# Kernel tuning notes

Hardware: AMD Instinct MI355X
Metric: run time of the kernel (lower is better)

Reference implementation:

```python
import jax, jax.numpy as jnp
import numpy as np

SCALE = 0.08838834764831845  # 1/sqrt(128)
NEG_INF = -1e30


def setup_inputs() -> dict:
    key = jax.random.key(0)
    ks = jax.random.split(key, 6)
    S, Hq, Hkv, D, NB, BS, BMAX, X = 32, 32, 8, 128, 4096, 16, 128, 8
    query = jax.random.normal(ks[0], (S, Hq, D), jnp.float32)
    key_cache = jax.random.normal(ks[1], (NB, Hkv, D // X, BS, X), jnp.float32)
    value_cache = jax.random.normal(ks[2], (NB, Hkv, D, BS), jnp.float32)
    block_tables = jax.random.randint(ks[3], (S, BMAX), 0, NB, dtype=jnp.int32)
    seq_lens = jax.random.randint(ks[4], (S,), 1, BMAX * BS + 1, dtype=jnp.int32)
    alibi_slopes = jax.random.uniform(ks[5], (Hq,), jnp.float32)
    query_start_len = jnp.arange(S + 1, dtype=jnp.int32)  # every seq is a 1-token decode
    return dict(query_ptr=query, key_cache_ptr=key_cache, value_cache_ptr=value_cache,
                block_tables_ptr=block_tables, seq_lens_ptr=seq_lens,
                alibi_slopes_ptr=alibi_slopes, query_start_len_ptr=query_start_len)


def reference(query_ptr, key_cache_ptr, value_cache_ptr, block_tables_ptr,
              seq_lens_ptr, alibi_slopes_ptr, query_start_len_ptr):
    S, Bmax = block_tables_ptr.shape
    NB, Hkv, D0, BS, X = key_cache_ptr.shape
    D = D0 * X
    Hq = query_ptr.shape[1]
    G = Hq // Hkv  # queries per kv head
    Kmax = Bmax * BS

    # de-interleave vLLM K layout [NB,Hkv,D//x,BS,x] -> [NB,Hkv,BS,D]; K[d] = cache[.., d//x, tok, d%x]
    K = key_cache_ptr.transpose(0, 1, 3, 2, 4).reshape(NB, Hkv, BS, D).astype(jnp.float32)
    V = value_cache_ptr.transpose(0, 1, 3, 2).astype(jnp.float32)  # [NB,Hkv,BS,D]

    qstart = query_start_len_ptr[:-1]
    qlen = query_start_len_ptr[1:] - qstart

    q = query_ptr[qstart].astype(jnp.float32).reshape(S, Hkv, G, D)  # one decode token per seq

    # block-table-driven KV gather: [S,Bmax,Hkv,BS,D] -> [S,Hkv,Kmax,D]
    Kg = K[block_tables_ptr].transpose(0, 2, 1, 3, 4).reshape(S, Hkv, Kmax, D)
    Vg = V[block_tables_ptr].transpose(0, 2, 1, 3, 4).reshape(S, Hkv, Kmax, D)

    scores = SCALE * jnp.einsum('shgd,shkd->shgk', q, Kg)  # [S,Hkv,G,Kmax]

    pos = jnp.arange(Kmax, dtype=jnp.float32)
    ctx = (seq_lens_ptr.astype(jnp.float32) - 1.0)[:, None, None, None]
    slopes = alibi_slopes_ptr.reshape(Hkv, G)  # head idx = kv_head*G + q
    bias = slopes[None, :, :, None] * (pos[None, None, None, :] - ctx)
    valid = (jnp.arange(Kmax)[None, :] < seq_lens_ptr[:, None])[:, None, None, :]
    scores = jnp.where(valid, scores + bias, NEG_INF)

    m = jnp.max(scores, axis=-1, keepdims=True)
    p = jnp.exp(scores - m) * valid  # online-softmax numerator
    l = jnp.sum(p, axis=-1, keepdims=True)
    acc = jnp.einsum('shgk,shkd->shgd', p, Vg)
    out = acc / (l + 1e-10)  # matches acc/(L + 1e-10) in source

    decode = (qlen == 1).astype(query_ptr.dtype)  # seqs with query_len>1 are skipped (zeros)
    out = out.reshape(S, Hq, D).astype(query_ptr.dtype) * decode[:, None, None]
    return jnp.zeros_like(query_ptr).at[qstart].set(out)
```

## Files before the change

kernel.cpp:

```cpp
#include <hip/hip_runtime.h>

#define SCALE_F 0.08838834764831845f
#define NEG_INF -1e30f

constexpr int S    = 32;
constexpr int Hq   = 32;
constexpr int Hkv  = 8;
constexpr int G    = 4;
constexpr int D    = 128;
constexpr int BS   = 16;
constexpr int BMAX = 128;
constexpr int KMAX = BMAX * BS;

template<int PARTS>
__global__ __launch_bounds__(256, 4)
void attn_wave_kernel(const float* __restrict__ q_ptr,
                      const float* __restrict__ kc,
                      const float* __restrict__ vc,
                      const int*   __restrict__ bt,
                      const int*   __restrict__ slens,
                      const float* __restrict__ slopes,
                      float* __restrict__ part_acc,
                      float* __restrict__ part_m,
                      float* __restrict__ part_l)
{
    constexpr int CHUNKW = KMAX / PARTS;
    constexpr int NCH    = CHUNKW / 64;
    constexpr int CPW    = CHUNKW / BS;

    __shared__ float sm_p[4][G * CHUNKW];

    const int wid  = threadIdx.x >> 6;
    const int lane = threadIdx.x & 63;
    const int gw   = blockIdx.x * 4 + wid;
    const int part = gw % PARTS;
    const int sh   = gw / PARTS;
    const int h    = sh & (Hkv - 1);
    const int s    = sh >> 3;

    const int seq_len   = slens[s];
    const int num_parts = (seq_len + CHUNKW - 1) / CHUNKW;
    if (part >= num_parts) return;

    float* smp = sm_p[wid];

    int phys[CPW];
    #pragma unroll
    for (int i = 0; i < CPW; ++i) phys[i] = bt[s * BMAX + part * CPW + i];

    const float ctx  = (float)(seq_len - 1);
    const int   pos0 = part * CHUNKW;

    const int o4 = lane >> 4;
    const int t  = lane & 15;

    const float wslope = slopes[h * G + (t & 3)];

    float4 qa[G], qb[G];
    #pragma unroll
    for (int g = 0; g < G; ++g) {
        const float* qp = q_ptr + ((size_t)(s * Hq + h * G + g) * D + t * 8);
        qa[g] = ((const float4*)qp)[0];
        qb[g] = ((const float4*)qp)[1];
    }

    #pragma unroll
    for (int c = 0; c < NCH; ++c) {
        #pragma unroll
        for (int jb = 0; jb < 4; ++jb) {
            const float* kbase = kc + ((((size_t)phys[c * 4 + jb] * Hkv + h) * (D / 8) + t) * BS) * 8;
            float4 kA[4], kB[4];
            #pragma unroll
            for (int j2 = 0; j2 < 4; ++j2) {
                const float* kp = kbase + (j2 * 4 + o4) * 8;
                kA[j2] = ((const float4*)kp)[0];
                kB[j2] = ((const float4*)kp)[1];
            }
            #pragma unroll
            for (int j2 = 0; j2 < 4; ++j2) {
                float sc0 = qa[0].x*kA[j2].x + qa[0].y*kA[j2].y + qa[0].z*kA[j2].z + qa[0].w*kA[j2].w
                          + qb[0].x*kB[j2].x + qb[0].y*kB[j2].y + qb[0].z*kB[j2].z + qb[0].w*kB[j2].w;
                float sc1 = qa[1].x*kA[j2].x + qa[1].y*kA[j2].y + qa[1].z*kA[j2].z + qa[1].w*kA[j2].w
                          + qb[1].x*kB[j2].x + qb[1].y*kB[j2].y + qb[1].z*kB[j2].z + qb[1].w*kB[j2].w;
                float sc2 = qa[2].x*kA[j2].x + qa[2].y*kA[j2].y + qa[2].z*kA[j2].z + qa[2].w*kA[j2].w
                          + qb[2].x*kB[j2].x + qb[2].y*kB[j2].y + qb[2].z*kB[j2].z + qb[2].w*kB[j2].w;
                float sc3 = qa[3].x*kA[j2].x + qa[3].y*kA[j2].y + qa[3].z*kA[j2].z + qa[3].w*kA[j2].w
                          + qb[3].x*kB[j2].x + qb[3].y*kB[j2].y + qb[3].z*kB[j2].z + qb[3].w*kB[j2].w;
                #pragma unroll
                for (int msk = 8; msk >= 1; msk >>= 1) {
                    sc0 += __shfl_xor(sc0, msk, 16);
                    sc1 += __shfl_xor(sc1, msk, 16);
                    sc2 += __shfl_xor(sc2, msk, 16);
                    sc3 += __shfl_xor(sc3, msk, 16);
                }
                if (t < 4) {
                    const int pl   = c * 64 + (jb * 4 + j2) * 4 + o4;
                    const int kpos = pos0 + pl;
                    const float scv = (t == 0) ? sc0 : (t == 1) ? sc1 : (t == 2) ? sc2 : sc3;
                    smp[t * CHUNKW + pl] =
                        (kpos < seq_len) ? (SCALE_F * scv + wslope * ((float)kpos - ctx)) : NEG_INF;
                }
            }
        }
    }

    const int d0 = lane;
    float4 vreg[2][2][4];
    {
        const float* vb = vc + ((size_t)phys[0] * Hkv + h) * D * BS;
        #pragma unroll
        for (int c = 0; c < 4; ++c) {
            vreg[0][0][c] = ((const float4*)(vb + (size_t)d0 * BS))[c];
            vreg[0][1][c] = ((const float4*)(vb + (size_t)(d0 + 64) * BS))[c];
        }
    }

    {
        const int gS = lane >> 4;
        const int u  = lane & 15;
        float* rowp = smp + gS * CHUNKW;

        float4 sv[NCH];
        float m = NEG_INF;
        #pragma unroll
        for (int w = 0; w < NCH; ++w) {
            sv[w] = ((const float4*)(rowp + u * 4 + w * 64))[0];
            m = fmaxf(m, fmaxf(fmaxf(sv[w].x, sv[w].y), fmaxf(sv[w].z, sv[w].w)));
        }
        #pragma unroll
        for (int msk = 8; msk >= 1; msk >>= 1) m = fmaxf(m, __shfl_xor(m, msk, 16));

        float l = 0.f;
        #pragma unroll
        for (int w = 0; w < NCH; ++w) {
            float4 pv;
            pv.x = __expf(sv[w].x - m);
            pv.y = __expf(sv[w].y - m);
            pv.z = __expf(sv[w].z - m);
            pv.w = __expf(sv[w].w - m);
            l += pv.x + pv.y + pv.z + pv.w;
            ((float4*)(rowp + u * 4 + w * 64))[0] = pv;
        }
        #pragma unroll
        for (int msk = 8; msk >= 1; msk >>= 1) l += __shfl_xor(l, msk, 16);

        if (u == 0) {
            part_m[(sh * PARTS + part) * G + gS] = m;
            part_l[(sh * PARTS + part) * G + gS] = l;
        }
    }

    float acc0[G] = {0.f, 0.f, 0.f, 0.f};
    float acc1[G] = {0.f, 0.f, 0.f, 0.f};

    #pragma unroll
    for (int i = 0; i < CPW; ++i) {
        const int cb = i & 1;
        if (i + 1 < CPW) {
            const float* vb = vc + ((size_t)phys[i + 1] * Hkv + h) * D * BS;
            #pragma unroll
            for (int c = 0; c < 4; ++c) {
                vreg[cb ^ 1][0][c] = ((const float4*)(vb + (size_t)d0 * BS))[c];
                vreg[cb ^ 1][1][c] = ((const float4*)(vb + (size_t)(d0 + 64) * BS))[c];
            }
        }
        #pragma unroll
        for (int g = 0; g < G; ++g) {
            const float4* pp = (const float4*)(smp + g * CHUNKW + i * BS);
            #pragma unroll
            for (int c = 0; c < 4; ++c) {
                const float4 p4 = pp[c];
                acc0[g] += p4.x * vreg[cb][0][c].x + p4.y * vreg[cb][0][c].y
                         + p4.z * vreg[cb][0][c].z + p4.w * vreg[cb][0][c].w;
                acc1[g] += p4.x * vreg[cb][1][c].x + p4.y * vreg[cb][1][c].y
                         + p4.z * vreg[cb][1][c].z + p4.w * vreg[cb][1][c].w;
            }
        }
    }

    float* outp = part_acc + (size_t)(sh * PARTS + part) * G * D;
    #pragma unroll
    for (int g = 0; g < G; ++g) {
        outp[g * D + d0]      = acc0[g];
        outp[g * D + d0 + 64] = acc1[g];
    }
}

__global__ __launch_bounds__(512)
void attn_reduce_kernel(const float* __restrict__ part_acc,
                        const float* __restrict__ part_m,
                        const float* __restrict__ part_l,
                        const int*   __restrict__ slens,
                        float* __restrict__ out,
                        int parts, int chunk)
{
    const int sh  = blockIdx.x;
    const int s   = sh / Hkv;
    const int tid = threadIdx.x;
    const int g   = tid >> 7;
    const int d   = tid & 127;

    const int seq_len = slens[s];
    const int np = min(parts, (seq_len + chunk - 1) / chunk);

    float M = NEG_INF;
    for (int p = 0; p < np; ++p)
        M = fmaxf(M, part_m[(sh * parts + p) * G + g]);
    float L = 0.f, acc = 0.f;
    for (int p = 0; p < np; ++p) {
        const float w = __expf(part_m[(sh * parts + p) * G + g] - M);
        L += w * part_l[(sh * parts + p) * G + g];
        acc += w * part_acc[((size_t)(sh * parts + p) * G + g) * D + d];
    }
    out[(size_t)(sh * G + g) * D + d] = acc / (L + 1e-10f);
}

extern "C" void kernel_launch(void* const* d_in, const int* in_sizes, int n_in,
                              void* d_out, int out_size, void* d_ws, size_t ws_size,
                              hipStream_t stream)
{
    const float* q   = (const float*)d_in[0];
    const float* kc  = (const float*)d_in[1];
    const float* vc  = (const float*)d_in[2];
    const int*   bt  = (const int*)d_in[3];
    const int*   sl  = (const int*)d_in[4];
    const float* slp = (const float*)d_in[5];

    auto ws_need = [](int p) {
        return (size_t)S * Hkv * p * G * (D + 2) * sizeof(float);
    };
    int parts = 16;
    while (parts > 4 && ws_need(parts) > ws_size) parts >>= 1;
    const int chunk = KMAX / parts;

    float* part_acc = (float*)d_ws;
    float* part_m   = part_acc + (size_t)S * Hkv * parts * G * D;
    float* part_l   = part_m   + (size_t)S * Hkv * parts * G;

    const dim3 grid1(S * Hkv * parts / 4);
    switch (parts) {
    case 16: attn_wave_kernel<16><<<grid1, 256, 0, stream>>>(q, kc, vc, bt, sl, slp, part_acc, part_m, part_l); break;
    case 8:  attn_wave_kernel<8> <<<grid1, 256, 0, stream>>>(q, kc, vc, bt, sl, slp, part_acc, part_m, part_l); break;
    default: attn_wave_kernel<4> <<<grid1, 256, 0, stream>>>(q, kc, vc, bt, sl, slp, part_acc, part_m, part_l); break;
    }
    attn_reduce_kernel<<<S * Hkv, 512, 0, stream>>>(
        part_acc, part_m, part_l, sl, (float*)d_out, parts, chunk);
}
```

Before: 472.6 us.

## Double-buffer K block loads and split KV sequence into 32 partitions

The QK score loop now walks one 16-token cache block at a time and loads the next block's K vectors into a second register buffer while the current block is computed, so global-load latency overlaps with the FMAs. The default split count rises from 16 to 32, which gives 64-token chunks and twice as many wavefronts, to raise memory-level parallelism. The per-chunk softmax is simplified to read a single float4 per lane. The launch-bounds occupancy hint drops from 4 to 3 to leave room for the extra registers. The simplified softmax only covers 64-wide chunks, so the smaller-partition fallback paths would compute wrong results if workspace limits forced them.

```diff
diff --git a/kernel.cpp b/kernel.cpp
--- a/kernel.cpp
+++ b/kernel.cpp
@@ -13,7 +13,7 @@
 constexpr int KMAX = BMAX * BS;
 
 template<int PARTS>
-__global__ __launch_bounds__(256, 4)
+__global__ __launch_bounds__(256, 3)
 void attn_wave_kernel(const float* __restrict__ q_ptr,
                       const float* __restrict__ kc,
                       const float* __restrict__ vc,
@@ -25,7 +25,6 @@
                       float* __restrict__ part_l)
 {
     constexpr int CHUNKW = KMAX / PARTS;
-    constexpr int NCH    = CHUNKW / 64;
     constexpr int CPW    = CHUNKW / BS;
 
     __shared__ float sm_p[4][G * CHUNKW];
@@ -64,42 +63,52 @@
         qb[g] = ((const float4*)qp)[1];
     }
 
-    #pragma unroll
-    for (int c = 0; c < NCH; ++c) {
-        #pragma unroll
-        for (int jb = 0; jb < 4; ++jb) {
-            const float* kbase = kc + ((((size_t)phys[c * 4 + jb] * Hkv + h) * (D / 8) + t) * BS) * 8;
-            float4 kA[4], kB[4];
+    float4 kA[2][4], kB[2][4];
+    {
+        const float* kbase = kc + ((((size_t)phys[0] * Hkv + h) * (D / 8) + t) * BS) * 8;
+        #pragma unroll
+        for (int j2 = 0; j2 < 4; ++j2) {
+            const float* kp = kbase + (j2 * 4 + o4) * 8;
+            kA[0][j2] = ((const float4*)kp)[0];
+            kB[0][j2] = ((const float4*)kp)[1];
+        }
+    }
+
+    #pragma unroll
+    for (int i = 0; i < CPW; ++i) {
+        const int cb = i & 1;
+        if (i + 1 < CPW) {
+            const float* kbase = kc + ((((size_t)phys[i + 1] * Hkv + h) * (D / 8) + t) * BS) * 8;
             #pragma unroll
             for (int j2 = 0; j2 < 4; ++j2) {
                 const float* kp = kbase + (j2 * 4 + o4) * 8;
-                kA[j2] = ((const float4*)kp)[0];
-                kB[j2] = ((const float4*)kp)[1];
-            }
-            #pragma unroll
-            for (int j2 = 0; j2 < 4; ++j2) {
-                float sc0 = qa[0].x*kA[j2].x + qa[0].y*kA[j2].y + qa[0].z*kA[j2].z + qa[0].w*kA[j2].w
-                          + qb[0].x*kB[j2].x + qb[0].y*kB[j2].y + qb[0].z*kB[j2].z + qb[0].w*kB[j2].w;
-                float sc1 = qa[1].x*kA[j2].x + qa[1].y*kA[j2].y + qa[1].z*kA[j2].z + qa[1].w*kA[j2].w
-                          + qb[1].x*kB[j2].x + qb[1].y*kB[j2].y + qb[1].z*kB[j2].z + qb[1].w*kB[j2].w;
-                float sc2 = qa[2].x*kA[j2].x + qa[2].y*kA[j2].y + qa[2].z*kA[j2].z + qa[2].w*kA[j2].w
-                          + qb[2].x*kB[j2].x + qb[2].y*kB[j2].y + qb[2].z*kB[j2].z + qb[2].w*kB[j2].w;
-                float sc3 = qa[3].x*kA[j2].x + qa[3].y*kA[j2].y + qa[3].z*kA[j2].z + qa[3].w*kA[j2].w
-                          + qb[3].x*kB[j2].x + qb[3].y*kB[j2].y + qb[3].z*kB[j2].z + qb[3].w*kB[j2].w;
-                #pragma unroll
-                for (int msk = 8; msk >= 1; msk >>= 1) {
-                    sc0 += __shfl_xor(sc0, msk, 16);
-                    sc1 += __shfl_xor(sc1, msk, 16);
-                    sc2 += __shfl_xor(sc2, msk, 16);
-                    sc3 += __shfl_xor(sc3, msk, 16);
-                }
-                if (t < 4) {
-                    const int pl   = c * 64 + (jb * 4 + j2) * 4 + o4;
-                    const int kpos = pos0 + pl;
-                    const float scv = (t == 0) ? sc0 : (t == 1) ? sc1 : (t == 2) ? sc2 : sc3;
-                    smp[t * CHUNKW + pl] =
-                        (kpos < seq_len) ? (SCALE_F * scv + wslope * ((float)kpos - ctx)) : NEG_INF;
-                }
+                kA[cb ^ 1][j2] = ((const float4*)kp)[0];
+                kB[cb ^ 1][j2] = ((const float4*)kp)[1];
+            }
+        }
+        #pragma unroll
+        for (int j2 = 0; j2 < 4; ++j2) {
+            float sc0 = qa[0].x*kA[cb][j2].x + qa[0].y*kA[cb][j2].y + qa[0].z*kA[cb][j2].z + qa[0].w*kA[cb][j2].w
+                      + qb[0].x*kB[cb][j2].x + qb[0].y*kB[cb][j2].y + qb[0].z*kB[cb][j2].z + qb[0].w*kB[cb][j2].w;
+            float sc1 = qa[1].x*kA[cb][j2].x + qa[1].y*kA[cb][j2].y + qa[1].z*kA[cb][j2].z + qa[1].w*kA[cb][j2].w
+                      + qb[1].x*kB[cb][j2].x + qb[1].y*kB[cb][j2].y + qb[1].z*kB[cb][j2].z + qb[1].w*kB[cb][j2].w;
+            float sc2 = qa[2].x*kA[cb][j2].x + qa[2].y*kA[cb][j2].y + qa[2].z*kA[cb][j2].z + qa[2].w*kA[cb][j2].w
+                      + qb[2].x*kB[cb][j2].x + qb[2].y*kB[cb][j2].y + qb[2].z*kB[cb][j2].z + qb[2].w*kB[cb][j2].w;
+            float sc3 = qa[3].x*kA[cb][j2].x + qa[3].y*kA[cb][j2].y + qa[3].z*kA[cb][j2].z + qa[3].w*kA[cb][j2].w
+                      + qb[3].x*kB[cb][j2].x + qb[3].y*kB[cb][j2].y + qb[3].z*kB[cb][j2].z + qb[3].w*kB[cb][j2].w;
+            #pragma unroll
+            for (int msk = 8; msk >= 1; msk >>= 1) {
+                sc0 += __shfl_xor(sc0, msk, 16);
+                sc1 += __shfl_xor(sc1, msk, 16);
+                sc2 += __shfl_xor(sc2, msk, 16);
+                sc3 += __shfl_xor(sc3, msk, 16);
+            }
+            if (t < 4) {
+                const int pl   = i * BS + j2 * 4 + o4;
+                const int kpos = pos0 + pl;
+                const float scv = (t == 0) ? sc0 : (t == 1) ? sc1 : (t == 2) ? sc2 : sc3;
+                smp[t * CHUNKW + pl] =
+                    (kpos < seq_len) ? (SCALE_F * scv + wslope * ((float)kpos - ctx)) : NEG_INF;
             }
         }
     }
@@ -120,27 +129,18 @@
         const int u  = lane & 15;
         float* rowp = smp + gS * CHUNKW;
 
-        float4 sv[NCH];
-        float m = NEG_INF;
-        #pragma unroll
-        for (int w = 0; w < NCH; ++w) {
-            sv[w] = ((const float4*)(rowp + u * 4 + w * 64))[0];
-            m = fmaxf(m, fmaxf(fmaxf(sv[w].x, sv[w].y), fmaxf(sv[w].z, sv[w].w)));
-        }
+        float4 sv = ((const float4*)(rowp + u * 4))[0];
+        float m = fmaxf(fmaxf(sv.x, sv.y), fmaxf(sv.z, sv.w));
         #pragma unroll
         for (int msk = 8; msk >= 1; msk >>= 1) m = fmaxf(m, __shfl_xor(m, msk, 16));
 
-        float l = 0.f;
-        #pragma unroll
-        for (int w = 0; w < NCH; ++w) {
-            float4 pv;
-            pv.x = __expf(sv[w].x - m);
-            pv.y = __expf(sv[w].y - m);
-            pv.z = __expf(sv[w].z - m);
-            pv.w = __expf(sv[w].w - m);
-            l += pv.x + pv.y + pv.z + pv.w;
-            ((float4*)(rowp + u * 4 + w * 64))[0] = pv;
-        }
+        float4 pv;
+        pv.x = __expf(sv.x - m);
+        pv.y = __expf(sv.y - m);
+        pv.z = __expf(sv.z - m);
+        pv.w = __expf(sv.w - m);
+        float l = pv.x + pv.y + pv.z + pv.w;
+        ((float4*)(rowp + u * 4))[0] = pv;
         #pragma unroll
         for (int msk = 8; msk >= 1; msk >>= 1) l += __shfl_xor(l, msk, 16);
 
@@ -229,7 +229,7 @@
     auto ws_need = [](int p) {
         return (size_t)S * Hkv * p * G * (D + 2) * sizeof(float);
     };
-    int parts = 16;
+    int parts = 32;
     while (parts > 4 && ws_need(parts) > ws_size) parts >>= 1;
     const int chunk = KMAX / parts;
 
@@ -239,6 +239,7 @@
 
     const dim3 grid1(S * Hkv * parts / 4);
     switch (parts) {
+    case 32: attn_wave_kernel<32><<<grid1, 256, 0, stream>>>(q, kc, vc, bt, sl, slp, part_acc, part_m, part_l); break;
     case 16: attn_wave_kernel<16><<<grid1, 256, 0, stream>>>(q, kc, vc, bt, sl, slp, part_acc, part_m, part_l); break;
     case 8:  attn_wave_kernel<8> <<<grid1, 256, 0, stream>>>(q, kc, vc, bt, sl, slp, part_acc, part_m, part_l); break;
     default: attn_wave_kernel<4> <<<grid1, 256, 0, stream>>>(q, kc, vc, bt, sl, slp, part_acc, part_m, part_l); break;
```

Result: slower. 483.5 us (+2.3%).
